# Optimization experiments

Hardware: AMD Instinct MI355X
Metric: run time of the kernel (lower is better)

The kernel has to match this reference:

```python
import jax, jax.numpy as jnp
import numpy as np

WINDOW_SIZE = 11
SIGMA = 1.5
C1 = 0.01 ** 2
C2 = 0.03 ** 2


def _gaussian_1d(window_size, sigma):
    x = np.arange(window_size, dtype=np.float32)
    g = np.exp(-((x - window_size // 2) ** 2) / (2.0 * sigma ** 2))
    g = g / g.sum()
    return jnp.asarray(g, dtype=jnp.float32)


def _blur(x, g1d):
    # Separable depthwise Gaussian blur, SAME padding.
    # x: [B, C, H, W]; mathematically identical to conv with outer(g, g).
    c = x.shape[1]
    pad = WINDOW_SIZE // 2
    kh = jnp.broadcast_to(g1d.reshape(1, 1, WINDOW_SIZE, 1), (c, 1, WINDOW_SIZE, 1))
    kw = jnp.broadcast_to(g1d.reshape(1, 1, 1, WINDOW_SIZE), (c, 1, 1, WINDOW_SIZE))
    dn = ('NCHW', 'OIHW', 'NCHW')
    x = jax.lax.conv_general_dilated(x, kh, (1, 1), [(pad, pad), (0, 0)],
                                     dimension_numbers=dn, feature_group_count=c)
    x = jax.lax.conv_general_dilated(x, kw, (1, 1), [(0, 0), (pad, pad)],
                                     dimension_numbers=dn, feature_group_count=c)
    return x


def setup_inputs() -> dict:
    key = jax.random.key(0)
    k1, k2 = jax.random.split(key)
    shape = (32, 1, 512, 512)
    img1 = jax.random.uniform(k1, shape, dtype=jnp.float32)
    img2 = jax.random.uniform(k2, shape, dtype=jnp.float32)
    return {"img1": img1, "img2": img2}


def reference(img1, img2):
    g1d = _gaussian_1d(WINDOW_SIZE, SIGMA)
    mu1 = _blur(img1, g1d)
    mu2 = _blur(img2, g1d)
    mu1_sq = mu1 * mu1
    mu2_sq = mu2 * mu2
    mu1_mu2 = mu1 * mu2
    sigma1_sq = _blur(img1 * img1, g1d) - mu1_sq
    sigma2_sq = _blur(img2 * img2, g1d) - mu2_sq
    sigma12 = _blur(img1 * img2, g1d) - mu1_mu2
    ssim_map = ((2.0 * mu1_mu2 + C1) * (2.0 * sigma12 + C2)) / (
        (mu1_sq + mu2_sq + C1) * (sigma1_sq + sigma2_sq + C2))
    return ssim_map.mean()  # size_average=True
```

## Files before the change

### kernel.cpp

```cpp
#include <hip/hip_runtime.h>

#define HH 512
#define WW 512
#define BATCH 32
#define BH 16
#define NB (HH / BH)
#define TPB 256
#define VTW 528
#define NBLOCKS (NB * BATCH)

struct WS {
  unsigned counter;
  unsigned pad;
  double accum;
};

__global__ void ssim_init(WS* w) {
  if (threadIdx.x == 0) { w->counter = 0u; w->accum = 0.0; }
}

__global__ __launch_bounds__(TPB, 4) void ssim_main(
    const float* __restrict__ img1,
    const float* __restrict__ img2,
    WS* __restrict__ ws,
    float* __restrict__ out)
{
  constexpr float G[11] = {
      0.00102838f, 0.00759876f, 0.03600077f, 0.10936070f, 0.21300553f,
      0.26601171f,
      0.21300553f, 0.10936070f, 0.03600077f, 0.00759876f, 0.00102838f};
  constexpr float C1 = 1.0e-4f;
  constexpr float C2 = 9.0e-4f;

  const int tid  = threadIdx.x;
  const int band = blockIdx.x;
  const int bat  = blockIdx.y;
  const int r0   = band * BH;
  const float* p1 = img1 + (size_t)bat * (HH * WW);
  const float* p2 = img2 + (size_t)bat * (HH * WW);
  const int c0 = tid * 2;

  __shared__ __align__(16) float vt[2][5][VTW];

  if (tid < 8) {
#pragma unroll
    for (int u = 0; u < 2; ++u)
#pragma unroll
      for (int a = 0; a < 5; ++a) {
        vt[u][a][tid]       = 0.f;
        vt[u][a][520 + tid] = 0.f;
      }
  }

  float2 w1[12], w2[12];
#pragma unroll
  for (int j = 0; j < 12; ++j) {
    const int r = r0 - 5 + j;
    float2 a = make_float2(0.f, 0.f), b = make_float2(0.f, 0.f);
    if (r >= 0 && r < HH) {
      a = *(const float2*)(p1 + r * WW + c0);
      b = *(const float2*)(p2 + r * WW + c0);
    }
    w1[j] = a;
    w2[j] = b;
  }

  __syncthreads();

  float ssum = 0.f;

#pragma unroll 1
  for (int q = 0; q < BH; q += 2) {
    float2 ta1 = make_float2(0.f, 0.f), ta2 = ta1, tb1 = ta1, tb2 = ta1;
    const bool pf = (q + 2 < BH);
    if (pf) {
      const int ra = r0 + 7 + q;
      const int rb = r0 + 8 + q;
      if (ra < HH) {
        ta1 = *(const float2*)(p1 + ra * WW + c0);
        ta2 = *(const float2*)(p2 + ra * WW + c0);
      }
      if (rb < HH) {
        tb1 = *(const float2*)(p1 + rb * WW + c0);
        tb2 = *(const float2*)(p2 + rb * WW + c0);
      }
    }

#pragma unroll
    for (int s = 0; s < 2; ++s) {
      float acc[5][2];
#pragma unroll
      for (int a = 0; a < 5; ++a) { acc[a][0] = 0.f; acc[a][1] = 0.f; }

#pragma unroll
      for (int k = 0; k < 11; ++k) {
        const float gk = G[k];
        const float2 a2 = w1[k + s];
        const float2 b2 = w2[k + s];
        const float av[2] = {a2.x, a2.y};
        const float bv[2] = {b2.x, b2.y};
#pragma unroll
        for (int i = 0; i < 2; ++i) {
          const float t1 = gk * av[i];
          const float t2 = gk * bv[i];
          acc[0][i] += t1;
          acc[1][i] += t2;
          acc[2][i] = fmaf(t1, av[i], acc[2][i]);
          acc[3][i] = fmaf(t2, bv[i], acc[3][i]);
          acc[4][i] = fmaf(t1, bv[i], acc[4][i]);
        }
      }

#pragma unroll
      for (int a = 0; a < 5; ++a) {
        ((float2*)(&vt[s][a][0]))[4 + tid] = make_float2(acc[a][0], acc[a][1]);
      }

      __syncthreads();

      float h[5][2];
#pragma unroll
      for (int a = 0; a < 5; ++a) {
        const float2* r2 = (const float2*)(&vt[s][a][0]);
        float x[14];
#pragma unroll
        for (int m = 0; m < 7; ++m) {
          const float2 v = r2[tid + 1 + m];
          x[2 * m]     = v.x;
          x[2 * m + 1] = v.y;
        }
#pragma unroll
        for (int j = 0; j < 2; ++j) {
          float hv = 0.f;
#pragma unroll
          for (int k = 0; k < 11; ++k) hv = fmaf(G[k], x[j + k + 1], hv);
          h[a][j] = hv;
        }
      }

#pragma unroll
      for (int j = 0; j < 2; ++j) {
        const float mu1 = h[0][j], mu2 = h[1][j];
        const float mu12 = mu1 * mu2;
        const float mu1s = mu1 * mu1;
        const float mu2s = mu2 * mu2;
        const float sg1  = h[2][j] - mu1s;
        const float sg2  = h[3][j] - mu2s;
        const float sg12 = h[4][j] - mu12;
        const float num = (2.f * mu12 + C1) * (2.f * sg12 + C2);
        const float den = (mu1s + mu2s + C1) * (sg1 + sg2 + C2);
        ssum += num / den;
      }
    }

#pragma unroll
    for (int j = 0; j < 10; ++j) { w1[j] = w1[j + 2]; w2[j] = w2[j + 2]; }
    w1[10] = ta1; w2[10] = ta2;
    w1[11] = tb1; w2[11] = tb2;
  }

#pragma unroll
  for (int off = 32; off > 0; off >>= 1) ssum += __shfl_xor(ssum, off, 64);
  __shared__ float wsum[4];
  if ((tid & 63) == 0) wsum[tid >> 6] = ssum;
  __syncthreads();
  if (tid == 0) {
    const float bsum = wsum[0] + wsum[1] + wsum[2] + wsum[3];
    atomicAdd(&ws->accum, (double)bsum);
    __threadfence();
    const unsigned old = atomicAdd(&ws->counter, 1u);
    if (old == NBLOCKS - 1) {
      const double tot = atomicAdd(&ws->accum, 0.0);
      out[0] = (float)(tot / (double)((size_t)BATCH * HH * WW));
    }
  }
}

extern "C" void kernel_launch(void* const* d_in, const int* in_sizes, int n_in,
                              void* d_out, int out_size, void* d_ws, size_t ws_size,
                              hipStream_t stream) {
  const float* img1 = (const float*)d_in[0];
  const float* img2 = (const float*)d_in[1];
  float* out = (float*)d_out;
  WS* ws = (WS*)d_ws;
  ssim_init<<<1, 64, 0, stream>>>(ws);
  dim3 grid(NB, BATCH);
  ssim_main<<<grid, TPB, 0, stream>>>(img1, img2, ws, out);
}
```

Measured before the change: 134.7 us.

## Make each wavefront self-contained with halo columns to drop block barriers

Each 64-lane wavefront now owns a 128-column strip and computes its own 5-column halos on either side by redundantly vertical-blurring extra columns in lanes 0-9. This lets the horizontal pass read only wave-private shared memory, so the two __syncthreads per row pair become wave barriers plus an LDS waitcnt. The aim is to remove block-wide synchronization stalls. In exchange there is redundant vertical work in 10 lanes, extra scalar global loads, and more registers. The init kernel is also replaced with hipMemsetAsync.

```diff
diff --git a/kernel.cpp b/kernel.cpp
--- a/kernel.cpp
+++ b/kernel.cpp
@@ -6,18 +6,14 @@
 #define BH 16
 #define NB (HH / BH)
 #define TPB 256
-#define VTW 528
 #define NBLOCKS (NB * BATCH)
+#define HSW 144
 
 struct WS {
   unsigned counter;
   unsigned pad;
   double accum;
 };
-
-__global__ void ssim_init(WS* w) {
-  if (threadIdx.x == 0) { w->counter = 0u; w->accum = 0.0; }
-}
 
 __global__ __launch_bounds__(TPB, 4) void ssim_main(
     const float* __restrict__ img1,
@@ -33,64 +29,71 @@
   constexpr float C2 = 9.0e-4f;
 
   const int tid  = threadIdx.x;
+  const int lane = tid & 63;
+  const int wv   = tid >> 6;
   const int band = blockIdx.x;
   const int bat  = blockIdx.y;
   const int r0   = band * BH;
   const float* p1 = img1 + (size_t)bat * (HH * WW);
   const float* p2 = img2 + (size_t)bat * (HH * WW);
-  const int c0 = tid * 2;
-
-  __shared__ __align__(16) float vt[2][5][VTW];
-
-  if (tid < 8) {
-#pragma unroll
-    for (int u = 0; u < 2; ++u)
-#pragma unroll
-      for (int a = 0; a < 5; ++a) {
-        vt[u][a][tid]       = 0.f;
-        vt[u][a][520 + tid] = 0.f;
-      }
-  }
+
+  const int cb = wv * 128;
+  const int c0 = cb + 2 * lane;
+
+  const int  hrel  = (lane < 5) ? (lane - 5) : (lane + 123);
+  const int  hcol  = cb + hrel;
+  const bool hlane = (lane < 10);
+  const bool hok   = hlane && (hcol >= 0) && (hcol < WW);
+  const int  hp    = hrel + 6;
+
+  __shared__ __align__(16) float hs[4][2][5][HSW];
+  __shared__ float wsum[4];
 
   float2 w1[12], w2[12];
+  float  e1[12], e2[12];
 #pragma unroll
   for (int j = 0; j < 12; ++j) {
     const int r = r0 - 5 + j;
-    float2 a = make_float2(0.f, 0.f), b = make_float2(0.f, 0.f);
+    float2 a = make_float2(0.f, 0.f), b = a;
+    float  ea = 0.f, eb = 0.f;
     if (r >= 0 && r < HH) {
       a = *(const float2*)(p1 + r * WW + c0);
       b = *(const float2*)(p2 + r * WW + c0);
-    }
-    w1[j] = a;
-    w2[j] = b;
+      if (hok) {
+        ea = p1[r * WW + hcol];
+        eb = p2[r * WW + hcol];
+      }
+    }
+    w1[j] = a; w2[j] = b; e1[j] = ea; e2[j] = eb;
   }
-
-  __syncthreads();
 
   float ssum = 0.f;
 
 #pragma unroll 1
   for (int q = 0; q < BH; q += 2) {
+    const int ra = r0 + 7 + q;
+    const int rb = r0 + 8 + q;
     float2 ta1 = make_float2(0.f, 0.f), ta2 = ta1, tb1 = ta1, tb2 = ta1;
-    const bool pf = (q + 2 < BH);
-    if (pf) {
-      const int ra = r0 + 7 + q;
-      const int rb = r0 + 8 + q;
-      if (ra < HH) {
-        ta1 = *(const float2*)(p1 + ra * WW + c0);
-        ta2 = *(const float2*)(p2 + ra * WW + c0);
-      }
-      if (rb < HH) {
-        tb1 = *(const float2*)(p1 + rb * WW + c0);
-        tb2 = *(const float2*)(p2 + rb * WW + c0);
-      }
-    }
+    float  tea1 = 0.f, tea2 = 0.f, teb1 = 0.f, teb2 = 0.f;
+    if (ra < HH) {
+      ta1 = *(const float2*)(p1 + ra * WW + c0);
+      ta2 = *(const float2*)(p2 + ra * WW + c0);
+      if (hok) { tea1 = p1[ra * WW + hcol]; tea2 = p2[ra * WW + hcol]; }
+    }
+    if (rb < HH) {
+      tb1 = *(const float2*)(p1 + rb * WW + c0);
+      tb2 = *(const float2*)(p2 + rb * WW + c0);
+      if (hok) { teb1 = p1[rb * WW + hcol]; teb2 = p2[rb * WW + hcol]; }
+    }
+
+    __builtin_amdgcn_wave_barrier();
 
 #pragma unroll
     for (int s = 0; s < 2; ++s) {
       float acc[5][2];
-#pragma unroll
-      for (int a = 0; a < 5; ++a) { acc[a][0] = 0.f; acc[a][1] = 0.f; }
+      float hacc[5];
+#pragma unroll
+      for (int a = 0; a < 5; ++a) { acc[a][0] = 0.f; acc[a][1] = 0.f; hacc[a] = 0.f; }
 
 #pragma unroll
       for (int k = 0; k < 11; ++k) {
@@ -109,23 +112,38 @@
           acc[3][i] = fmaf(t2, bv[i], acc[3][i]);
           acc[4][i] = fmaf(t1, bv[i], acc[4][i]);
         }
+        const float he1 = e1[k + s];
+        const float he2 = e2[k + s];
+        const float t1 = gk * he1;
+        const float t2 = gk * he2;
+        hacc[0] += t1;
+        hacc[1] += t2;
+        hacc[2] = fmaf(t1, he1, hacc[2]);
+        hacc[3] = fmaf(t2, he2, hacc[3]);
+        hacc[4] = fmaf(t1, he2, hacc[4]);
       }
 
 #pragma unroll
       for (int a = 0; a < 5; ++a) {
-        ((float2*)(&vt[s][a][0]))[4 + tid] = make_float2(acc[a][0], acc[a][1]);
-      }
-
-      __syncthreads();
-
+        ((float2*)(&hs[wv][s][a][0]))[lane + 3] = make_float2(acc[a][0], acc[a][1]);
+        if (hlane) hs[wv][s][a][hp] = hacc[a];
+      }
+    }
+
+    __builtin_amdgcn_wave_barrier();
+    __builtin_amdgcn_s_waitcnt(0xC07F);
+    __builtin_amdgcn_wave_barrier();
+
+#pragma unroll
+    for (int s = 0; s < 2; ++s) {
       float h[5][2];
 #pragma unroll
       for (int a = 0; a < 5; ++a) {
-        const float2* r2 = (const float2*)(&vt[s][a][0]);
+        const float2* r2 = (const float2*)(&hs[wv][s][a][0]);
         float x[14];
 #pragma unroll
         for (int m = 0; m < 7; ++m) {
-          const float2 v = r2[tid + 1 + m];
+          const float2 v = r2[lane + m];
           x[2 * m]     = v.x;
           x[2 * m + 1] = v.y;
         }
@@ -154,15 +172,17 @@
     }
 
 #pragma unroll
-    for (int j = 0; j < 10; ++j) { w1[j] = w1[j + 2]; w2[j] = w2[j + 2]; }
-    w1[10] = ta1; w2[10] = ta2;
-    w1[11] = tb1; w2[11] = tb2;
+    for (int j = 0; j < 10; ++j) {
+      w1[j] = w1[j + 2]; w2[j] = w2[j + 2];
+      e1[j] = e1[j + 2]; e2[j] = e2[j + 2];
+    }
+    w1[10] = ta1; w2[10] = ta2; e1[10] = tea1; e2[10] = tea2;
+    w1[11] = tb1; w2[11] = tb2; e1[11] = teb1; e2[11] = teb2;
   }
 
 #pragma unroll
   for (int off = 32; off > 0; off >>= 1) ssum += __shfl_xor(ssum, off, 64);
-  __shared__ float wsum[4];
-  if ((tid & 63) == 0) wsum[tid >> 6] = ssum;
+  if (lane == 0) wsum[wv] = ssum;
   __syncthreads();
   if (tid == 0) {
     const float bsum = wsum[0] + wsum[1] + wsum[2] + wsum[3];
@@ -183,7 +203,7 @@
   const float* img2 = (const float*)d_in[1];
   float* out = (float*)d_out;
   WS* ws = (WS*)d_ws;
-  ssim_init<<<1, 64, 0, stream>>>(ws);
+  hipMemsetAsync(ws, 0, 16, stream);
   dim3 grid(NB, BATCH);
   ssim_main<<<grid, TPB, 0, stream>>>(img1, img2, ws, out);
 }
```

New measurement: 282.7 us. 2.1x slower.
